# Kernel optimization log

Measured on AMD Instinct MI355X. Metric: run time of the kernel, lower is better.

Reference implementation:

```python
import jax, jax.numpy as jnp
import numpy as np

K = 9
HEADS = 4

def _inorm(x, axes):
    # torch InstanceNorm (affine=False, eps=1e-5, biased variance)
    m = x.mean(axes, keepdims=True)
    v = ((x - m) ** 2).mean(axes, keepdims=True)
    return (x - m) * jax.lax.rsqrt(v + 1e-5)

def _lrelu(x):
    return jax.nn.leaky_relu(x, 0.2)

def _knn_idx(coords, k):
    # coords: [B, 2, N] -> idx of k nearest (excluding self): [B, N, k]
    pts = jnp.swapaxes(coords, 1, 2)  # [B, N, 2]
    sq = (pts ** 2).sum(-1)
    dist = sq[:, :, None] + sq[:, None, :] - 2.0 * jnp.einsum('bnc,bmc->bnm', pts, pts)
    dist = jnp.maximum(dist, 1e-12)
    _, idx = jax.lax.top_k(-dist, k + 1)  # smallest distances, sorted
    return idx[:, :, 1:]

def _gather_nb(feats, idx):
    # feats: [B, C, N], idx: [B, N, k] -> [B, C, N, k]
    return jnp.take_along_axis(feats[:, :, None, :], idx[:, None, :, :], axis=3)

def _graph_feature(coords, feats, k):
    B, C, N = feats.shape
    idx = _knn_idx(coords, k)
    nb = _gather_nb(feats, idx)
    ctr = jnp.broadcast_to(feats[..., None], (B, C, N, k))
    return jnp.concatenate([ctr, nb - ctr], axis=1), idx  # [B, 2C, N, k]

def _annu(x, w1, b1, w2, b2):
    # conv (1,3) stride (1,3): non-overlapping windows 9 -> 3, then conv (1,3): 3 -> 1
    B, Ci, N, kk = x.shape
    x = x.reshape(B, Ci, N, kk // 3, 3)
    x = jnp.einsum('bcnwt,oct->bonw', x, w1) + b1[None, :, None, None]
    x = jax.nn.relu(_inorm(x, (2, 3)))
    x = jnp.einsum('bcnt,oct->bon', x, w2) + b2[None, :, None]
    return jax.nn.relu(_inorm(x[..., None], (2, 3)))  # [B, Co, N, 1]

def _cos(a, b):
    dot = (a * b).sum(1)
    return (dot / (jnp.sqrt((a ** 2).sum(1)) * jnp.sqrt((b ** 2).sum(1))))[:, None]

def _self_attn(coords, feats, p):
    B, C, N = feats.shape
    k = min(K, N - 1)
    x0 = feats[..., None]
    x1_old, idx1 = _graph_feature(coords, feats, k)
    x1 = _annu(x1_old, p['a1w1'], p['a1b1'], p['a1w2'], p['a1b2'])
    ctr = jnp.broadcast_to(coords[..., None], coords.shape + (k,))  # [B,2,N,k]
    nei1 = _gather_nb(coords, idx1)
    f_ang1 = _annu(_cos(ctr, nei1), p['gw1'], p['gb1'], p['gw2'], p['gb2'])
    x2_cat, idx2 = _graph_feature(coords, x1[..., 0], k)
    x2 = _annu(x2_cat, p['a2w1'], p['a2b1'], p['a2w2'], p['a2b2'])
    nei2 = _gather_nb(coords, idx2)
    f_ang2 = _annu(_cos(ctr, nei2), p['gw1'], p['gb1'], p['gw2'], p['gb2'])
    x3 = jnp.concatenate([x0, x1 + f_ang1, x2 + f_ang2], axis=1)
    x3 = _lrelu(_inorm(jnp.einsum('oc,bcnk->bonk', p['conv3_w'], x3), (2, 3))).reshape(B, -1, N)
    x1o = _lrelu(_inorm(jnp.einsum('oc,bcnk->bonk', p['conv1_w'], x1_old), (2, 3))).max(-1, keepdims=True)
    x2o_cat, _ = _graph_feature(coords, x1o[..., 0], k)
    x2o = _lrelu(_inorm(jnp.einsum('oc,bcnk->bonk', p['conv2_w'], x2o_cat), (2, 3))).max(-1, keepdims=True)
    x3o = jnp.concatenate([x0, x1o, x2o], axis=1)
    x3o = _lrelu(_inorm(jnp.einsum('oc,bcnk->bonk', p['conv3o_w'], x3o), (2, 3))).reshape(B, -1, N)
    return x3 + x3o

def _mha(q_in, k_in, v_in, p):
    B, D, N = q_in.shape
    dim = D // HEADS
    def proj(x, w, b):
        return (jnp.einsum('oc,bcn->bon', w, x) + b[None, :, None]).reshape(B, dim, HEADS, -1)
    q = proj(q_in, p['wq'], p['bq'])
    kk = proj(k_in, p['wk'], p['bk'])
    v = proj(v_in, p['wv'], p['bv'])
    scores = jnp.einsum('bdhn,bdhm->bhnm', q, kk) / jnp.sqrt(jnp.float32(dim))
    prob = jax.nn.softmax(scores, axis=-1)
    x = jnp.einsum('bhnm,bdhm->bdhn', prob, v).reshape(B, D, -1)
    return jnp.einsum('oc,bcn->bon', p['wm'], x) + p['bm'][None, :, None]

def _attn_prop(x, source, p):
    msg = _mha(x, source, source, p)
    h = jnp.concatenate([x, msg], axis=1)
    h = jnp.einsum('oc,bcn->bon', p['mw1'], h) + p['mb1'][None, :, None]
    h = jax.nn.relu(_inorm(h, (2,)))
    return jnp.einsum('oc,bcn->bon', p['mw2'], h) + p['mb2'][None, :, None]

def setup_inputs() -> dict:
    key = jax.random.key(0)
    ks = iter(jax.random.split(key, 40))
    def rn(shape, s=0.1):
        return jax.random.normal(next(ks), shape, jnp.float32) * s
    B, C, N = 2, 128, 2048
    return {
        'desc0': rn((B, C, N), 1.0), 'desc1': rn((B, C, N), 1.0),
        'coords0': rn((B, 2, N), 1.0), 'coords1': rn((B, 2, N), 1.0),
        'sa_conv1_w': rn((C, 2 * C)), 'sa_conv2_w': rn((2 * C, 2 * C)),
        'sa_conv3_w': rn((C, 3 * C)), 'sa_conv3o_w': rn((C, 4 * C)),
        'sa_a1w1': rn((C, 2 * C, 3)), 'sa_a1b1': rn((C,)), 'sa_a1w2': rn((C, C, 3)), 'sa_a1b2': rn((C,)),
        'sa_a2w1': rn((C, 2 * C, 3)), 'sa_a2b1': rn((C,)), 'sa_a2w2': rn((C, C, 3)), 'sa_a2b2': rn((C,)),
        'sa_gw1': rn((C, 1, 3)), 'sa_gb1': rn((C,)), 'sa_gw2': rn((C, C, 3)), 'sa_gb2': rn((C,)),
        'ca_wq': rn((C, C)), 'ca_bq': rn((C,)), 'ca_wk': rn((C, C)), 'ca_bk': rn((C,)),
        'ca_wv': rn((C, C)), 'ca_bv': rn((C,)), 'ca_wm': rn((C, C)), 'ca_bm': rn((C,)),
        'ca_mw1': rn((2 * C, 2 * C)), 'ca_mb1': rn((2 * C,)), 'ca_mw2': rn((C, 2 * C)), 'ca_mb2': rn((C,)),
    }

def reference(desc0, desc1, coords0, coords1, sa_conv1_w, sa_conv2_w, sa_conv3_w, sa_conv3o_w, sa_a1w1, sa_a1b1, sa_a1w2, sa_a1b2, sa_a2w1, sa_a2b1, sa_a2w2, sa_a2b2, sa_gw1, sa_gb1, sa_gw2, sa_gb2, ca_wq, ca_bq, ca_wk, ca_bk, ca_wv, ca_bv, ca_wm, ca_bm, ca_mw1, ca_mb1, ca_mw2, ca_mb2):
    sp = dict(conv1_w=sa_conv1_w, conv2_w=sa_conv2_w, conv3_w=sa_conv3_w, conv3o_w=sa_conv3o_w,
              a1w1=sa_a1w1, a1b1=sa_a1b1, a1w2=sa_a1w2, a1b2=sa_a1b2,
              a2w1=sa_a2w1, a2b1=sa_a2b1, a2w2=sa_a2w2, a2b2=sa_a2b2,
              gw1=sa_gw1, gb1=sa_gb1, gw2=sa_gw2, gb2=sa_gb2)
    cp = dict(wq=ca_wq, bq=ca_bq, wk=ca_wk, bk=ca_bk, wv=ca_wv, bv=ca_bv, wm=ca_wm, bm=ca_bm,
              mw1=ca_mw1, mb1=ca_mb1, mw2=ca_mw2, mb2=ca_mb2)
    # layer_names = ['self', 'cross']
    desc0 = _self_attn(coords0, desc0, sp)
    desc1 = _self_attn(coords1, desc1, sp)
    desc0 = desc0 + _attn_prop(desc0, desc1, cp)
    desc1 = desc1 + _attn_prop(desc1, desc0, cp)
    return (desc0, desc1)
```

## Files before the change

### kernel.cpp

```cpp
#include <hip/hip_runtime.h>
#include <cfloat>
#include <math.h>

#define NPTS 2048
#define R2   8192
#define SPLITK 8

typedef __attribute__((ext_vector_type(8))) short bfrag;
typedef __attribute__((ext_vector_type(4))) float f32x4;

__device__ inline ushort f2bf(float f) {
  unsigned u = __float_as_uint(f);
  return (ushort)((u + 0x7fffu + ((u >> 16) & 1u)) >> 16);
}

__global__ __launch_bounds__(256) void prologue(
    const float* __restrict__ conv1, const float* __restrict__ conv2,
    const float* __restrict__ a1w1, const float* __restrict__ a1w2,
    const float* __restrict__ a2w1, const float* __restrict__ a2w2,
    const float* __restrict__ gw2,
    const float* __restrict__ wk, const float* __restrict__ bk,
    const float* __restrict__ wv, const float* __restrict__ bv,
    float* __restrict__ dwA1, float* __restrict__ a1w2r,
    float* __restrict__ dwA2, float* __restrict__ a2w2r,
    float* __restrict__ gw2r, float* __restrict__ dwC1, float* __restrict__ dwC2,
    float* __restrict__ wkv, float* __restrict__ bkv,
    const float* __restrict__ in0, const float* __restrict__ in1, float* __restrict__ FT,
    const float* __restrict__ P0, const float* __restrict__ P1,
    int* __restrict__ idx, float* __restrict__ cosv)
{
  int bid = blockIdx.x, tid = threadIdx.x;
  if (bid < 256) {
    int i = bid * 256 + tid;
    if (i < 512*128) {
      int row = i >> 7, c = i & 127;
      float v1, v2;
      if (row < 128) {
        float s1 = 0.f, s2 = 0.f;
        for (int t = 0; t < 3; t++) {
          s1 += a1w1[(row*256 + c)*3 + t] - a1w1[(row*256 + 128 + c)*3 + t];
          s2 += a2w1[(row*256 + c)*3 + t] - a2w1[(row*256 + 128 + c)*3 + t];
        }
        v1 = s1; v2 = s2;
      } else {
        int t = (row - 128) >> 7, o = row & 127;
        v1 = a1w1[(o*256 + 128 + c)*3 + t];
        v2 = a2w1[(o*256 + 128 + c)*3 + t];
      }
      dwA1[i] = v1; dwA2[i] = v2;
      dwC2[i] = (row < 256) ? (conv2[row*256 + c] - conv2[row*256 + 128 + c])
                            : conv2[(row-256)*256 + 128 + c];
    }
    if (i < 128*384) {
      int o = i / 384, rem = i % 384, w = rem >> 7, c = rem & 127;
      a1w2r[i] = a1w2[(o*128 + c)*3 + w];
      a2w2r[i] = a2w2[(o*128 + c)*3 + w];
      gw2r[i]  = gw2[(o*128 + c)*3 + w];
    }
    if (i < 256*128) {
      int row = i >> 7, c = i & 127;
      dwC1[i] = (row < 128) ? (conv1[row*256 + c] - conv1[row*256 + 128 + c])
                            : conv1[(row-128)*256 + 128 + c];
      wkv[i] = (row < 128) ? wk[row*128 + c] : wv[(row-128)*128 + c];
    }
    if (i < 256) bkv[i] = (i < 128) ? bk[i] : bv[i - 128];
    return;
  }
  if (bid < 1280) {
    __shared__ float tile[32][33];
    int q = bid - 256;
    int zb = q >> 8, rem = q & 255, by = rem >> 6, bx = rem & 63;
    const float* src = (zb < 2) ? (in0 + (size_t)zb*128*2048) : (in1 + (size_t)(zb-2)*128*2048);
    float* dst = FT + (size_t)zb*2048*128;
    int i0 = by * 32, j0 = bx * 32;
    int tx = tid & 31, ty = tid >> 5;
    for (int s = 0; s < 32; s += 8)
      tile[ty + s][tx] = src[(size_t)(i0 + ty + s)*2048 + (j0 + tx)];
    __syncthreads();
    for (int s = 0; s < 32; s += 8)
      dst[(size_t)(j0 + ty + s)*128 + (i0 + tx)] = tile[tx][ty + s];
    return;
  }
  {
    __shared__ float px[NPTS], py[NPTS], sq[NPTS];
    int gw = (bid - 1280) * 4 + (tid >> 6);
    int b4 = gw >> 11, n = gw & 2047;
    int lane = tid & 63;
    const float* Pb = (b4 < 2) ? (P0 + (size_t)b4 * 2 * NPTS) : (P1 + (size_t)(b4 - 2) * 2 * NPTS);
    for (int i = tid; i < NPTS; i += 256) {
      float x = Pb[i], y = Pb[NPTS + i];
      px[i] = x; py[i] = y;
      sq[i] = __fadd_rn(__fmul_rn(x, x), __fmul_rn(y, y));
    }
    __syncthreads();
    float xn = px[n], yn = py[n], sqn = sq[n];
    float d32[32];
#pragma unroll
    for (int j = 0; j < 32; j++) {
      int m = lane + j*64;
      float dot  = __fadd_rn(__fmul_rn(xn, px[m]), __fmul_rn(yn, py[m]));
      float dist = __fsub_rn(__fadd_rn(sqn, sq[m]), __fmul_rn(2.0f, dot));
      d32[j] = fmaxf(dist, 1e-12f);
    }
    for (int r = 0; r < 10; r++) {
      float bv2 = d32[0]; int bj = 0;
#pragma unroll
      for (int j = 1; j < 32; j++) {
        bool lt = d32[j] < bv2;
        bv2 = lt ? d32[j] : bv2;
        bj = lt ? j : bj;
      }
      float wvv = bv2;
      int   wii = lane + bj*64;
      for (int off = 32; off >= 1; off >>= 1) {
        float od = __shfl_xor(wvv, off);
        int   oi = __shfl_xor(wii, off);
        if (od < wvv || (od == wvv && oi < wii)) { wvv = od; wii = oi; }
      }
      if (r > 0 && lane == 0) {
        size_t base = (size_t)gw*9 + (r - 1);
        idx[base] = wii;
        float dot = __fadd_rn(__fmul_rn(xn, px[wii]), __fmul_rn(yn, py[wii]));
        cosv[base] = __fdiv_rn(dot, __fmul_rn(__fsqrt_rn(sqn), __fsqrt_rn(sq[wii])));
      }
      if ((wii & 63) == lane) {
        int wj = wii >> 6;
#pragma unroll
        for (int j = 0; j < 32; j++) if (j == wj) d32[j] = FLT_MAX;
      }
    }
  }
}

__global__ void transpose_k(const float* __restrict__ in, float* __restrict__ out, int I, int J) {
  __shared__ float tile[32][33];
  int b = blockIdx.z;
  int i0 = blockIdx.y * 32, j0 = blockIdx.x * 32;
  int tx = threadIdx.x, ty = threadIdx.y;
  for (int s = 0; s < 32; s += 8)
    tile[ty + s][tx] = in[((size_t)b*I + (i0 + ty + s))*J + (j0 + tx)];
  __syncthreads();
  for (int s = 0; s < 32; s += 8)
    out[((size_t)b*J + (j0 + ty + s))*I + (i0 + tx)] = tile[tx][ty + s];
}

template<int BM>
__device__ __forceinline__ void gemm_body(
    const float* __restrict__ p0, int w0, const float* __restrict__ st0, int a0, int xm0,
    const float* __restrict__ p1, int w1, const float* __restrict__ st1, int a1, int xm1,
    const float* __restrict__ p2, int w2, const float* __restrict__ st2, int a2, int xm2,
    const float* __restrict__ addp, const float* __restrict__ addst,
    const float* __restrict__ W, const float* __restrict__ bias,
    const float* __restrict__ resid,
    float* __restrict__ Y, int Cin, int O, int pack, float* __restrict__ Y2,
    float* __restrict__ part,
    int r0, int c0, int pbx)
{
  __shared__ ushort Xs[BM][40];
  __shared__ ushort Ws[64][40];
  constexpr int RT = BM / 16;
  constexpr int XF = BM / 8;
  int tid = threadIdx.x;
  int wv = tid >> 6, l = tid & 63;
  int m16 = l & 15, kq = l >> 4;
  int sxr = tid & (BM - 1), sxc = (tid / BM) * XF;
  int swr = tid & 63, swc = (tid >> 6) * 8;
  f32x4 acc[RT];
#pragma unroll
  for (int t = 0; t < RT; t++) acc[t] = (f32x4){0.f, 0.f, 0.f, 0.f};
  for (int k0 = 0; k0 < Cin; k0 += 32) {
    {
      int r = r0 + sxr;
      int ac = k0 + sxc;
      const float* P; const float* st; int cc, lw, act, xm;
      if (ac < w0)            { P = p0; cc = ac;          lw = w0; st = st0; act = a0; xm = xm0; }
      else if (ac < w0 + w1)  { P = p1; cc = ac - w0;     lw = w1; st = st1; act = a1; xm = xm1; }
      else                    { P = p2; cc = ac - w0 - w1; lw = w2; st = st2; act = a2; xm = xm2; }
      float vv[XF];
#pragma unroll
      for (int q = 0; q < XF; q += 4)
        *(float4*)&vv[q] = *(const float4*)(P + (size_t)r*lw + cc + q);
      int b = r >> 11;
      if (st) {
#pragma unroll
        for (int j = 0; j < XF; j++) {
          int o = (cc + j) & (xm - 1);
          float m = st[(b*xm + o)*2], rs = st[(b*xm + o)*2 + 1];
          float v = (vv[j] - m) * rs;
          vv[j] = (act == 1) ? fmaxf(v, 0.f) : ((v >= 0.f) ? v : 0.2f*v);
        }
      }
      if (addp && ac >= 128) {
        int fc = (ac - 128) & 127;
        float av[XF];
#pragma unroll
        for (int q = 0; q < XF; q += 4)
          *(float4*)&av[q] = *(const float4*)(addp + (size_t)r*128 + fc + q);
        if (addst) {
#pragma unroll
          for (int j = 0; j < XF; j++) {
            int o = (fc + j) & 127;
            float m = addst[(b*128 + o)*2], rs = addst[(b*128 + o)*2 + 1];
            av[j] = fmaxf((av[j] - m) * rs, 0.f);
          }
        }
#pragma unroll
        for (int j = 0; j < XF; j++) vv[j] += av[j];
      }
      union { ushort u[XF]; ushort4 v4[XF/4]; } pk;
#pragma unroll
      for (int j = 0; j < XF; j++) pk.u[j] = f2bf(vv[j]);
#pragma unroll
      for (int q = 0; q < XF/4; q++) *(ushort4*)&Xs[sxr][sxc + q*4] = pk.v4[q];
    }
    {
      const float* s = W + (size_t)(c0 + swr)*Cin + k0 + swc;
      float4 v0 = *(const float4*)s, v1 = *(const float4*)(s + 4);
      union { ushort u[8]; ushort4 v4[2]; } pk;
      pk.u[0]=f2bf(v0.x); pk.u[1]=f2bf(v0.y); pk.u[2]=f2bf(v0.z); pk.u[3]=f2bf(v0.w);
      pk.u[4]=f2bf(v1.x); pk.u[5]=f2bf(v1.y); pk.u[6]=f2bf(v1.z); pk.u[7]=f2bf(v1.w);
      *(ushort4*)&Ws[swr][swc]     = pk.v4[0];
      *(ushort4*)&Ws[swr][swc + 4] = pk.v4[1];
    }
    __syncthreads();
    bfrag bf = *(const bfrag*)&Ws[wv*16 + m16][kq*8];
#pragma unroll
    for (int t = 0; t < RT; t++) {
      bfrag af = *(const bfrag*)&Xs[t*16 + m16][kq*8];
      acc[t] = __builtin_amdgcn_mfma_f32_16x16x32_bf16(af, bf, acc[t], 0, 0, 0);
    }
    __syncthreads();
  }
  int c = c0 + wv*16 + m16;
  float bi = bias ? bias[c] : 0.f;
  float ps = 0.f, ps2 = 0.f;
#pragma unroll
  for (int t = 0; t < RT; t++) {
#pragma unroll
    for (int i = 0; i < 4; i++) {
      int r = r0 + t*16 + kq*4 + i;
      float v = acc[t][i] + bi;
      if (resid) v += resid[(size_t)r*O + c];
      if (pack) {
        int cc2 = c & 127;
        int h = cc2 & 3, dd = cc2 >> 2, b = r >> 11, n = r & 2047;
        float* T = (pack == 1 || c < 128) ? Y : Y2;
        T[(((size_t)(b*4 + h))*NPTS + n)*32 + dd] = v;
      } else {
        Y[(size_t)r*O + c] = v;
      }
      ps += v; ps2 = fmaf(v, v, ps2);
    }
  }
  if (part) {
    ps  += __shfl_xor(ps, 16);  ps  += __shfl_xor(ps, 32);
    ps2 += __shfl_xor(ps2, 16); ps2 += __shfl_xor(ps2, 32);
    if (kq == 0) {
      part[((size_t)pbx*O + c)*2]     = ps;
      part[((size_t)pbx*O + c)*2 + 1] = ps2;
    }
  }
}

template<int BM>
__global__ __launch_bounds__(256) void gemm_m(
    const float* __restrict__ p0, int w0, const float* __restrict__ st0, int a0, int xm0,
    const float* __restrict__ p1, int w1, const float* __restrict__ st1, int a1, int xm1,
    const float* __restrict__ p2, int w2, const float* __restrict__ st2, int a2, int xm2,
    const float* __restrict__ addp, const float* __restrict__ addst,
    const float* __restrict__ W, const float* __restrict__ bias,
    const float* __restrict__ resid,
    float* __restrict__ Y, int Cin, int O, int pack, float* __restrict__ Y2,
    float* __restrict__ part)
{
  gemm_body<BM>(p0,w0,st0,a0,xm0, p1,w1,st1,a1,xm1, p2,w2,st2,a2,xm2,
                addp,addst, W,bias,resid, Y,Cin,O,pack,Y2,part,
                blockIdx.x*BM, blockIdx.y*64, blockIdx.x);
}

__global__ __launch_bounds__(256) void gemm_qkv(
    const float* __restrict__ Xbase,
    const float* __restrict__ wq, const float* __restrict__ bq, float* __restrict__ Qo,
    const float* __restrict__ wkv, const float* __restrict__ bkv, float* __restrict__ Ko,
    float* __restrict__ Vo)
{
  int bx = blockIdx.x, by = blockIdx.y;
  if (bx < 128) {
    if (by >= 2) return;
    gemm_body<32>(Xbase,128,nullptr,0,0, nullptr,0,nullptr,0,0, nullptr,0,nullptr,0,0,
                  nullptr,nullptr, wq, bq, nullptr, Qo, 128, 128, 1, nullptr, nullptr,
                  bx*32, by*64, 0);
  } else {
    gemm_body<32>(Xbase + (size_t)4096*128,128,nullptr,0,0, nullptr,0,nullptr,0,0, nullptr,0,nullptr,0,0,
                  nullptr,nullptr, wkv, bkv, nullptr, Ko, 128, 256, 2, Vo, nullptr,
                  (bx-128)*32, by*64, 0);
  }
}

__global__ __launch_bounds__(256) void combine_annu(const float* __restrict__ GA, const int* __restrict__ idx,
                                                    const float* __restrict__ b1, float* __restrict__ A,
                                                    double* __restrict__ part) {
  int t = threadIdx.x;
  int o = t & 127, sub = t >> 7;
  int r0 = blockIdx.x * 4;
  __shared__ int nbs[4][9];
  if (t < 36) nbs[t / 9][t % 9] = idx[(size_t)(r0 + t/9)*9 + (t % 9)];
  __syncthreads();
  float bo = b1[o];
  double s = 0.0, s2 = 0.0;
  for (int rr = sub; rr < 4; rr += 2) {
    int r = r0 + rr, rb = r & ~2047;
    float ctr = GA[(size_t)r*512 + o] + bo;
#pragma unroll
    for (int w = 0; w < 3; w++) {
      float acc = ctr;
#pragma unroll
      for (int t3 = 0; t3 < 3; t3++) {
        int m = nbs[rr][w*3 + t3];
        acc += GA[(size_t)(rb + m)*512 + 128 + t3*128 + o];
      }
      A[(size_t)r*384 + w*128 + o] = acc;
      s += (double)acc; s2 += (double)acc * (double)acc;
    }
  }
  __shared__ double ls[256], ls2[256];
  ls[t] = s; ls2[t] = s2;
  __syncthreads();
  if (sub == 0) {
    s += ls[128 + o]; s2 += ls2[128 + o];
    part[((size_t)blockIdx.x*128 + o)*2] = s;
    part[((size_t)blockIdx.x*128 + o)*2 + 1] = s2;
  }
}

__global__ __launch_bounds__(256) void stats_cos(const float* __restrict__ partf, float* __restrict__ stat,
                                                 const float* __restrict__ cosv, const float* __restrict__ gw1,
                                                 const float* __restrict__ gb1, float* __restrict__ ANG,
                                                 double* __restrict__ part2) {
  int bid = blockIdx.x, t = threadIdx.x;
  if (bid < 64) {
    int g = bid * 8 + (t >> 5);
    int lane = t & 31;
    if (g >= 512) return;
    int b = g >> 7, o = g & 127;
    double S = 0.0, S2 = 0.0;
    for (int u = lane; u < 64; u += 32) {
      size_t blk = (size_t)(b*64 + u);
      S  += (double)partf[(blk*128 + o)*2];
      S2 += (double)partf[(blk*128 + o)*2 + 1];
    }
    for (int off = 16; off >= 1; off >>= 1) {
      S  += __shfl_down(S, off, 32);
      S2 += __shfl_down(S2, off, 32);
    }
    if (lane == 0) {
      double mean = S / 2048;
      double var = S2 / 2048 - mean*mean;
      if (var < 0.0) var = 0.0;
      stat[g*2] = (float)mean;
      stat[g*2 + 1] = (float)(1.0 / sqrt(var + 1e-5));
    }
    return;
  }
  {
    int cbid = bid - 64;
    int o = t & 127, sub = t >> 7;
    int r0 = cbid * 16;
    float g0 = gw1[o*3], g1 = gw1[o*3+1], g2 = gw1[o*3+2], gb = gb1[o];
    __shared__ float cs[16][12];
    for (int i = t; i < 16*9; i += 256) cs[i / 9][i % 9] = cosv[(size_t)(r0 + i/9)*9 + (i % 9)];
    __syncthreads();
    double s = 0.0, s2 = 0.0;
    for (int rr = sub; rr < 16; rr += 2) {
      int r = r0 + rr;
#pragma unroll
      for (int w = 0; w < 3; w++) {
        float acc = gb;
        acc += cs[rr][w*3+0]*g0;
        acc += cs[rr][w*3+1]*g1;
        acc += cs[rr][w*3+2]*g2;
        ANG[(size_t)r*384 + w*128 + o] = acc;
        s += (double)acc; s2 += (double)acc * (double)acc;
      }
    }
    __shared__ double ls[256], ls2[256];
    ls[t] = s; ls2[t] = s2;
    __syncthreads();
    if (sub == 0) {
      s += ls[128 + o]; s2 += ls2[128 + o];
      part2[((size_t)cbid*128 + o)*2] = s;
      part2[((size_t)cbid*128 + o)*2 + 1] = s2;
    }
  }
}

__global__ __launch_bounds__(256) void gm_final(const double* __restrict__ part, float* __restrict__ stats,
                                                int Cc, int NB, int nblk, int count) {
  int g = blockIdx.x * 8 + (threadIdx.x >> 5);
  int lane = threadIdx.x & 31;
  if (g >= NB*Cc) return;
  int b = g / Cc, o = g % Cc;
  double S = 0.0, S2 = 0.0;
  for (int u = lane; u < nblk; u += 32) {
    size_t blk = (size_t)(b*nblk + u);
    S  += part[(blk*Cc + o)*2];
    S2 += part[(blk*Cc + o)*2 + 1];
  }
  for (int off = 16; off >= 1; off >>= 1) {
    S  += __shfl_down(S, off, 32);
    S2 += __shfl_down(S2, off, 32);
  }
  if (lane == 0) {
    double mean = S / count;
    double var = S2 / count - mean*mean;
    if (var < 0.0) var = 0.0;
    stats[g*2] = (float)mean;
    stats[g*2 + 1] = (float)(1.0 / sqrt(var + 1e-5));
  }
}

__global__ __launch_bounds__(256) void gm_final_f(const float* __restrict__ part, float* __restrict__ stats,
                                                  int Cc, int NB, int nblk, int count) {
  int g = blockIdx.x * 8 + (threadIdx.x >> 5);
  int lane = threadIdx.x & 31;
  if (g >= NB*Cc) return;
  int b = g / Cc, o = g % Cc;
  double S = 0.0, S2 = 0.0;
  for (int u = lane; u < nblk; u += 32) {
    size_t blk = (size_t)(b*nblk + u);
    S  += (double)part[(blk*Cc + o)*2];
    S2 += (double)part[(blk*Cc + o)*2 + 1];
  }
  for (int off = 16; off >= 1; off >>= 1) {
    S  += __shfl_down(S, off, 32);
    S2 += __shfl_down(S2, off, 32);
  }
  if (lane == 0) {
    double mean = S / count;
    double var = S2 / count - mean*mean;
    if (var < 0.0) var = 0.0;
    stats[g*2] = (float)mean;
    stats[g*2 + 1] = (float)(1.0 / sqrt(var + 1e-5));
  }
}

__global__ __launch_bounds__(256) void gather_max_partial(const float* __restrict__ G, const int* __restrict__ idx,
                                                          float* __restrict__ maxbuf, double* __restrict__ part,
                                                          int Cc) {
  int t = threadIdx.x;
  int o = t % Cc, sub = t / Cc, nsub = 256 / Cc;
  int r0 = blockIdx.x * 4;
  __shared__ int nbs[4][9];
  if (t < 36) nbs[t / 9][t % 9] = idx[(size_t)(r0 + t/9)*9 + (t % 9)];
  __syncthreads();
  double s = 0.0, s2 = 0.0;
  for (int rr = sub; rr < 4; rr += nsub) {
    int r = r0 + rr, rb = r & ~2047;
    float g = G[(size_t)r*2*Cc + o];
    float mx = -3.4e38f;
#pragma unroll
    for (int k = 0; k < 9; k++) {
      int m = nbs[rr][k];
      float v = g + G[(size_t)(rb + m)*2*Cc + Cc + o];
      mx = fmaxf(mx, v); s += (double)v; s2 += (double)v*(double)v;
    }
    maxbuf[(size_t)r*Cc + o] = mx;
  }
  if (nsub == 2) {
    __shared__ double ls[256], ls2[256];
    ls[t] = s; ls2[t] = s2;
    __syncthreads();
    if (sub == 0) { s += ls[Cc + o]; s2 += ls2[Cc + o]; }
  }
  if (sub == 0) {
    part[((size_t)blockIdx.x*Cc + o)*2] = s;
    part[((size_t)blockIdx.x*Cc + o)*2 + 1] = s2;
  }
}

__global__ void norm_add2(const float* __restrict__ src, float* __restrict__ dst,
                          const float* __restrict__ stats,
                          const float* __restrict__ addend, const float* __restrict__ astats,
                          int total) {
  int i = blockIdx.x * 256 + threadIdx.x;
  if (i >= total) return;
  int o = i & 127;
  int b = i >> 18;
  float m = stats[(b*128 + o)*2], rs = stats[(b*128 + o)*2 + 1];
  float v = (src[i] - m) * rs;
  v = (v >= 0.f) ? v : 0.2f*v;
  float ma = astats[(b*128 + o)*2], rsa = astats[(b*128 + o)*2 + 1];
  float a = (addend[i] - ma) * rsa;
  a = (a >= 0.f) ? a : 0.2f*a;
  dst[i] = v + a;
}

__global__ __launch_bounds__(256) void attn_part(const float* __restrict__ Qp, const float* __restrict__ Kp,
                                                 const float* __restrict__ Vp,
                                                 float* __restrict__ OP, float* __restrict__ ML) {
  __shared__ ushort Ks[64][40];
  __shared__ ushort Vt[32][72];
  __shared__ ushort Pb[64][72];
  int tid = threadIdx.x;
  int wv = tid >> 6, l = tid & 63;
  int d = l & 15, g = l >> 4;
  int kp = blockIdx.y, bh = blockIdx.z;
  int q0 = blockIdx.x * 64;
  const float* Qh = Qp + (size_t)bh * NPTS * 32;
  const float* Kh = Kp + (size_t)bh * NPTS * 32;
  const float* Vh = Vp + (size_t)bh * NPTS * 32;
  {
    int r = tid >> 2, c8 = (tid & 3) * 8;
    const float* q = Qh + (size_t)(q0 + r)*32 + c8;
    float4 v0 = *(const float4*)q, v1 = *(const float4*)(q + 4);
    union { ushort u[8]; ushort4 v4[2]; } pk;
    pk.u[0]=f2bf(v0.x); pk.u[1]=f2bf(v0.y); pk.u[2]=f2bf(v0.z); pk.u[3]=f2bf(v0.w);
    pk.u[4]=f2bf(v1.x); pk.u[5]=f2bf(v1.y); pk.u[6]=f2bf(v1.z); pk.u[7]=f2bf(v1.w);
    *(ushort4*)&Pb[r][c8]     = pk.v4[0];
    *(ushort4*)&Pb[r][c8 + 4] = pk.v4[1];
  }
  __syncthreads();
  bfrag qf = *(const bfrag*)&Pb[wv*16 + d][g*8];
  f32x4 Oc[2];
  Oc[0] = (f32x4){0.f,0.f,0.f,0.f}; Oc[1] = (f32x4){0.f,0.f,0.f,0.f};
  float m_[4] = {-FLT_MAX, -FLT_MAX, -FLT_MAX, -FLT_MAX};
  float l_[4] = {0.f, 0.f, 0.f, 0.f};
  const float sc = 0.17677669529663687f;
  int ks0 = kp * (NPTS / SPLITK);
  for (int k0 = ks0; k0 < ks0 + NPTS/SPLITK; k0 += 64) {
    __syncthreads();
    {
      int r = tid >> 2, c8 = (tid & 3) * 8;
      const float* kr = Kh + (size_t)(k0 + r)*32 + c8;
      float4 a0 = *(const float4*)kr, a1 = *(const float4*)(kr + 4);
      union { ushort u[8]; ushort4 v4[2]; } pk;
      pk.u[0]=f2bf(a0.x); pk.u[1]=f2bf(a0.y); pk.u[2]=f2bf(a0.z); pk.u[3]=f2bf(a0.w);
      pk.u[4]=f2bf(a1.x); pk.u[5]=f2bf(a1.y); pk.u[6]=f2bf(a1.z); pk.u[7]=f2bf(a1.w);
      *(ushort4*)&Ks[r][c8]     = pk.v4[0];
      *(ushort4*)&Ks[r][c8 + 4] = pk.v4[1];
      int vr = tid & 63, vd = (tid >> 6) * 8;
      const float* vp = Vh + (size_t)(k0 + vr)*32 + vd;
      float4 b0 = *(const float4*)vp, b1 = *(const float4*)(vp + 4);
      Vt[vd+0][vr] = f2bf(b0.x); Vt[vd+1][vr] = f2bf(b0.y);
      Vt[vd+2][vr] = f2bf(b0.z); Vt[vd+3][vr] = f2bf(b0.w);
      Vt[vd+4][vr] = f2bf(b1.x); Vt[vd+5][vr] = f2bf(b1.y);
      Vt[vd+6][vr] = f2bf(b1.z); Vt[vd+7][vr] = f2bf(b1.w);
    }
    __syncthreads();
    f32x4 S[4];
#pragma unroll
    for (int c = 0; c < 4; c++) {
      S[c] = (f32x4){0.f,0.f,0.f,0.f};
      bfrag kf = *(const bfrag*)&Ks[c*16 + d][g*8];
      S[c] = __builtin_amdgcn_mfma_f32_16x16x32_bf16(qf, kf, S[c], 0, 0, 0);
    }
    float cf[4];
#pragma unroll
    for (int i = 0; i < 4; i++) {
      float tm = fmaxf(fmaxf(S[0][i], S[1][i]), fmaxf(S[2][i], S[3][i])) * sc;
      for (int off = 1; off < 16; off <<= 1) tm = fmaxf(tm, __shfl_xor(tm, off));
      float mn = fmaxf(m_[i], tm);
      cf[i] = __expf(m_[i] - mn);
      m_[i] = mn;
    }
    float rs[4] = {0.f, 0.f, 0.f, 0.f};
    ushort pu[4][4];
#pragma unroll
    for (int c = 0; c < 4; c++)
#pragma unroll
      for (int i = 0; i < 4; i++) {
        float p = __expf(fmaf(S[c][i], sc, -m_[i]));
        rs[i] += p;
        pu[c][i] = f2bf(p);
      }
#pragma unroll
    for (int i = 0; i < 4; i++) {
      float r2 = rs[i];
      for (int off = 1; off < 16; off <<= 1) r2 += __shfl_xor(r2, off);
      l_[i] = l_[i]*cf[i] + r2;
      Oc[0][i] *= cf[i]; Oc[1][i] *= cf[i];
    }
#pragma unroll
    for (int c = 0; c < 4; c++)
#pragma unroll
      for (int i = 0; i < 4; i++)
        Pb[wv*16 + g*4 + i][c*16 + d] = pu[c][i];
#pragma unroll
    for (int s5 = 0; s5 < 2; s5++) {
      bfrag pf = *(const bfrag*)&Pb[wv*16 + d][g*8 + 32*s5];
#pragma unroll
      for (int td = 0; td < 2; td++) {
        union { ushort4 v4[2]; bfrag f; } vu;
        vu.v4[0] = *(const ushort4*)&Vt[td*16 + d][g*8 + 32*s5];
        vu.v4[1] = *(const ushort4*)&Vt[td*16 + d][g*8 + 32*s5 + 4];
        Oc[td] = __builtin_amdgcn_mfma_f32_16x16x32_bf16(pf, vu.f, Oc[td], 0, 0, 0);
      }
    }
  }
  size_t pb = (size_t)(kp*8 + bh) * NPTS;
#pragma unroll
  for (int i = 0; i < 4; i++) {
    int n = q0 + wv*16 + g*4 + i;
    OP[(pb + n)*32 + d]      = Oc[0][i];
    OP[(pb + n)*32 + 16 + d] = Oc[1][i];
    if (d == 0) { ML[(pb + n)*2] = m_[i]; ML[(pb + n)*2 + 1] = l_[i]; }
  }
}

__global__ void attn_merge(const float* __restrict__ OP, const float* __restrict__ ML,
                           float* __restrict__ out) {
  int i = blockIdx.x * 256 + threadIdx.x;
  if (i >= 8*2048*16) return;
  int dp = (i & 15) * 2;
  int n  = (i >> 4) & 2047;
  int bh = i >> 15;
  float mv[SPLITK], lv[SPLITK];
  float mm = -FLT_MAX;
#pragma unroll
  for (int p = 0; p < SPLITK; p++) {
    size_t pp = ((size_t)(p*8 + bh) * NPTS + n);
    mv[p] = ML[pp*2]; lv[p] = ML[pp*2 + 1];
    mm = fmaxf(mm, mv[p]);
  }
  float L = 0.f, ox = 0.f, oy = 0.f;
#pragma unroll
  for (int p = 0; p < SPLITK; p++) {
    size_t pp = ((size_t)(p*8 + bh) * NPTS + n);
    float w = __expf(mv[p] - mm);
    L += w * lv[p];
    float2 o = *(const float2*)&OP[pp*32 + dp];
    ox += w * o.x; oy += w * o.y;
  }
  float inv = 1.f / L;
  int b = bh >> 2, h = bh & 3;
  out[((size_t)(b*NPTS + n))*128 + (dp+0)*4 + h] = ox * inv;
  out[((size_t)(b*NPTS + n))*128 + (dp+1)*4 + h] = oy * inv;
}

extern "C" void kernel_launch(void* const* d_in, const int* in_sizes, int n_in,
                              void* d_out, int out_size, void* d_ws, size_t ws_size,
                              hipStream_t stream) {
  (void)in_sizes; (void)n_in; (void)out_size; (void)ws_size;
  const float* desc0  = (const float*)d_in[0];
  const float* desc1  = (const float*)d_in[1];
  const float* coords0= (const float*)d_in[2];
  const float* coords1= (const float*)d_in[3];
  const float* conv1w = (const float*)d_in[4];
  const float* conv2w = (const float*)d_in[5];
  const float* conv3w = (const float*)d_in[6];
  const float* conv3ow= (const float*)d_in[7];
  const float* a1w1 = (const float*)d_in[8];
  const float* a1b1 = (const float*)d_in[9];
  const float* a1w2 = (const float*)d_in[10];
  const float* a1b2 = (const float*)d_in[11];
  const float* a2w1 = (const float*)d_in[12];
  const float* a2b1 = (const float*)d_in[13];
  const float* a2w2 = (const float*)d_in[14];
  const float* a2b2 = (const float*)d_in[15];
  const float* gw1  = (const float*)d_in[16];
  const float* gb1  = (const float*)d_in[17];
  const float* gw2  = (const float*)d_in[18];
  const float* gb2  = (const float*)d_in[19];
  const float* wq = (const float*)d_in[20]; const float* bq = (const float*)d_in[21];
  const float* wk = (const float*)d_in[22]; const float* bk = (const float*)d_in[23];
  const float* wv = (const float*)d_in[24]; const float* bv = (const float*)d_in[25];
  const float* wm = (const float*)d_in[26]; const float* bm = (const float*)d_in[27];
  const float* mw1 = (const float*)d_in[28]; const float* mb1 = (const float*)d_in[29];
  const float* mw2 = (const float*)d_in[30]; const float* mb2 = (const float*)d_in[31];

  float* ws = (float*)d_ws;
  size_t off = 0;
  auto alloc = [&](size_t nel) { size_t r = off; off += (nel + 63) & ~(size_t)63; return r; };
  float* DW_A1 = ws + alloc(512*128);
  float* W_A1R = ws + alloc(128*384);
  float* DW_A2 = ws + alloc(512*128);
  float* W_A2R = ws + alloc(128*384);
  float* W_G2R = ws + alloc(128*384);
  float* DW_C1 = ws + alloc(256*128);
  float* DW_C2 = ws + alloc(512*128);
  float* W_KV  = ws + alloc(256*128);
  float* B_KV  = ws + alloc(256);
  float* SA   = ws + alloc((size_t)R2*128);
  float* XF0  = ws + alloc((size_t)4096*128);
  float* XF1  = ws + alloc((size_t)4096*128);
  int*   IDX  = (int*)(ws + alloc((size_t)R2*9));
  float* COSV = ws + alloc((size_t)R2*9);
  float* FT   = ws + alloc((size_t)R2*128);
  float* BIG  = ws + alloc((size_t)R2*512);
  float* ABUF = ws + alloc((size_t)R2*384);
  float* X1B  = ws + alloc((size_t)R2*128);
  float* FANG = ws + alloc((size_t)R2*128);
  float* X2B  = ws + alloc((size_t)R2*128);
  float* X3A  = ws + alloc((size_t)R2*128);
  float* X1O  = ws + alloc((size_t)R2*128);
  float* AB2  = ws + alloc((size_t)R2*256);
  float* X3O  = ws + alloc((size_t)R2*128);
  double* PART = (double*)(ws + alloc((size_t)2048*256*2*2));
  float*  PARTF = (float*)PART;
  double* PART2 = PART + (size_t)512*1024;
  float* STATS = ws + alloc(8*2048);
  float* MLB  = ws + alloc((size_t)SPLITK*8*NPTS*2);
  float* ST_T   = STATS;
  float* ST_X1B = STATS + 2048;
  float* ST_FANG= STATS + 4096;
  float* ST_X2B = STATS + 6144;
  float* ST_X3A = STATS + 8192;
  float* ST_X1O = STATS + 10240;
  float* ST_AB  = STATS + 12288;
  float* ST_X3O = STATS + 14336;
  float* OP  = BIG;

  auto g64 = [&](const float* p0,int w0,const float* st0,int a0,int x0,
                 const float* p1,int w1,const float* st1,int a1,int x1,
                 const float* p2,int w2,const float* st2,int a2,int x2,
                 const float* addp,const float* addst,
                 const float* W,const float* bias,const float* resid,
                 float* Y,int R,int Cin,int O,int pack,float* Y2,float* part) {
    gemm_m<64><<<dim3(R/64, O/64), 256, 0, stream>>>(p0,w0,st0,a0,x0, p1,w1,st1,a1,x1,
        p2,w2,st2,a2,x2, addp,addst, W,bias,resid, Y,Cin,O,pack,Y2,part);
  };
  auto g32 = [&](const float* p0,int w0,const float* st0,int a0,int x0,
                 const float* p1,int w1,const float* st1,int a1,int x1,
                 const float* p2,int w2,const float* st2,int a2,int x2,
                 const float* addp,const float* addst,
                 const float* W,const float* bias,const float* resid,
                 float* Y,int R,int Cin,int O,int pack,float* Y2,float* part) {
    gemm_m<32><<<dim3(R/32, O/64), 256, 0, stream>>>(p0,w0,st0,a0,x0, p1,w1,st1,a1,x1,
        p2,w2,st2,a2,x2, addp,addst, W,bias,resid, Y,Cin,O,pack,Y2,part);
  };
  auto statsF = [&](float* stat, int O, int NB, int nblk, int count) {
    gm_final_f<<<(NB*O + 7)/8, 256, 0, stream>>>(PARTF, stat, O, NB, nblk, count);
  };
  auto statsD = [&](float* stat, int O, int NB, int nblk, int count) {
    gm_final<<<(NB*O + 7)/8, 256, 0, stream>>>(PART, stat, O, NB, nblk, count);
  };
  auto gathermax = [&](const float* G, float* mx, int Cc, float* stat) {
    gather_max_partial<<<R2/4, 256, 0, stream>>>(G, IDX, mx, PART, Cc);
    statsD(stat, Cc, 4, 512, 2048*9);
  };

  prologue<<<3328, 256, 0, stream>>>(conv1w, conv2w, a1w1, a1w2, a2w1, a2w2, gw2,
                                     wk, bk, wv, bv,
                                     DW_A1, W_A1R, DW_A2, W_A2R, W_G2R, DW_C1, DW_C2,
                                     W_KV, B_KV,
                                     desc0, desc1, FT,
                                     coords0, coords1, IDX, COSV);

  g64(FT,128,nullptr,0,0, nullptr,0,nullptr,0,0, nullptr,0,nullptr,0,0, nullptr,nullptr,
      DW_A1, nullptr, nullptr, BIG, R2, 128, 512, 0, nullptr, nullptr);
  combine_annu<<<R2/4, 256, 0, stream>>>(BIG, IDX, a1b1, ABUF, PART);
  statsD(ST_T, 128, 4, 512, 2048*3);
  g32(ABUF,384,ST_T,1,128, nullptr,0,nullptr,0,0, nullptr,0,nullptr,0,0, nullptr,nullptr,
      W_A1R, a1b2, nullptr, X1B, R2, 384, 128, 0, nullptr, PARTF);
  stats_cos<<<64 + R2/16, 256, 0, stream>>>(PARTF, ST_X1B, COSV, gw1, gb1, ABUF, PART2);
  gm_final<<<(4*128 + 7)/8, 256, 0, stream>>>(PART2, ST_T, 128, 4, 128, 2048*3);
  g32(ABUF,384,ST_T,1,128, nullptr,0,nullptr,0,0, nullptr,0,nullptr,0,0, nullptr,nullptr,
      W_G2R, gb2, nullptr, FANG, R2, 384, 128, 0, nullptr, PARTF);
  statsF(ST_FANG, 128, 4, 64, 2048);
  g64(X1B,128,ST_X1B,1,128, nullptr,0,nullptr,0,0, nullptr,0,nullptr,0,0, nullptr,nullptr,
      DW_A2, nullptr, nullptr, BIG, R2, 128, 512, 0, nullptr, nullptr);
  combine_annu<<<R2/4, 256, 0, stream>>>(BIG, IDX, a2b1, ABUF, PART);
  statsD(ST_T, 128, 4, 512, 2048*3);
  g32(ABUF,384,ST_T,1,128, nullptr,0,nullptr,0,0, nullptr,0,nullptr,0,0, nullptr,nullptr,
      W_A2R, a2b2, nullptr, X2B, R2, 384, 128, 0, nullptr, PARTF);
  statsF(ST_X2B, 128, 4, 64, 2048);
  g32(FT,128,nullptr,0,0, X1B,128,ST_X1B,1,128, X2B,128,ST_X2B,1,128, FANG,ST_FANG,
      conv3w, nullptr, nullptr, X3A, R2, 384, 128, 0, nullptr, PARTF);
  statsF(ST_X3A, 128, 4, 64, 2048);
  g64(FT,128,nullptr,0,0, nullptr,0,nullptr,0,0, nullptr,0,nullptr,0,0, nullptr,nullptr,
      DW_C1, nullptr, nullptr, BIG, R2, 128, 256, 0, nullptr, nullptr);
  gathermax(BIG, X1O, 128, ST_X1O);
  g64(X1O,128,ST_X1O,2,128, nullptr,0,nullptr,0,0, nullptr,0,nullptr,0,0, nullptr,nullptr,
      DW_C2, nullptr, nullptr, BIG, R2, 128, 512, 0, nullptr, nullptr);
  gathermax(BIG, AB2, 256, ST_AB);
  g32(FT,128,nullptr,0,0, X1O,128,ST_X1O,2,128, AB2,256,ST_AB,2,256, nullptr,nullptr,
      conv3ow, nullptr, nullptr, X3O, R2, 512, 128, 0, nullptr, PARTF);
  statsF(ST_X3O, 128, 4, 64, 2048);
  norm_add2<<<(R2*128 + 255)/256, 256, 0, stream>>>(X3O, SA, ST_X3O, X3A, ST_X3A, R2*128);

  float* SA1 = SA + (size_t)4096*128;
  auto prop = [&](const float* xbase, float* dst) {
    const float* xin = xbase;
    gemm_qkv<<<dim3(256, 4), 256, 0, stream>>>(xbase, wq, bq, X1B, W_KV, B_KV, X2B, X3A);
    attn_part<<<dim3(2048/64, SPLITK, 8), 256, 0, stream>>>(X1B, X2B, X3A, OP, MLB);
    attn_merge<<<(8*2048*16 + 255)/256, 256, 0, stream>>>(OP, MLB, FANG);
    g32(FANG,128,nullptr,0,0, nullptr,0,nullptr,0,0, nullptr,0,nullptr,0,0, nullptr,nullptr,
        wm, bm, nullptr, X1O, 4096, 128, 128, 0, nullptr, nullptr);
    g32(xin,128,nullptr,0,0, X1O,128,nullptr,0,0, nullptr,0,nullptr,0,0, nullptr,nullptr,
        mw1, mb1, nullptr, ABUF, 4096, 256, 256, 0, nullptr, PARTF);
    statsF(ST_T, 256, 2, 64, 2048);
    g32(ABUF,256,ST_T,1,256, nullptr,0,nullptr,0,0, nullptr,0,nullptr,0,0, nullptr,nullptr,
        mw2, mb2, xin, dst, 4096, 256, 128, 0, nullptr, nullptr);
  };

  prop(SA, XF0);
  prop(SA1, XF1);

  transpose_k<<<dim3(128/32, 2048/32, 2), dim3(32, 8), 0, stream>>>(XF0, (float*)d_out, 2048, 128);
  transpose_k<<<dim3(128/32, 2048/32, 2), dim3(32, 8), 0, stream>>>(XF1, (float*)d_out + (size_t)4096*128, 2048, 128);
}
```

Baseline: 468.0 us.

## Fuse norm-stat finalization into GEMM epilogue and streamline kNN argmin

Each GEMM that produces per-block partial sums now finalizes the instance-norm mean and rstd itself. It does this with a last-block-done atomic counter, which removes the separate gm_final_f and stats launches. The kNN selection keeps each lane's running minimum and rescans its 32 registers only in the lane that owned the extracted winner, instead of every lane rescanning every round. The two output transposes merge into one launch, and stats_cos is reduced to a cos_conv kernel followed by the generic stats reduction. In exchange, the stats reduction runs on a single trailing block with serial per-thread loops, and the code adds counter memsets and threadfence overhead.

```diff
diff --git a/kernel.cpp b/kernel.cpp
--- a/kernel.cpp
+++ b/kernel.cpp
@@ -102,14 +102,14 @@
       float dist = __fsub_rn(__fadd_rn(sqn, sq[m]), __fmul_rn(2.0f, dot));
       d32[j] = fmaxf(dist, 1e-12f);
     }
+    float bv2 = d32[0]; int bj = 0;
+#pragma unroll
+    for (int j = 1; j < 32; j++) {
+      bool lt = d32[j] < bv2;
+      bv2 = lt ? d32[j] : bv2;
+      bj = lt ? j : bj;
+    }
     for (int r = 0; r < 10; r++) {
-      float bv2 = d32[0]; int bj = 0;
-#pragma unroll
-      for (int j = 1; j < 32; j++) {
-        bool lt = d32[j] < bv2;
-        bv2 = lt ? d32[j] : bv2;
-        bj = lt ? j : bj;
-      }
       float wvv = bv2;
       int   wii = lane + bj*64;
       for (int off = 32; off >= 1; off >>= 1) {
@@ -127,6 +127,13 @@
         int wj = wii >> 6;
 #pragma unroll
         for (int j = 0; j < 32; j++) if (j == wj) d32[j] = FLT_MAX;
+        bv2 = d32[0]; bj = 0;
+#pragma unroll
+        for (int j = 1; j < 32; j++) {
+          bool lt = d32[j] < bv2;
+          bv2 = lt ? d32[j] : bv2;
+          bj = lt ? j : bj;
+        }
       }
     }
   }
@@ -154,7 +161,8 @@
     const float* __restrict__ resid,
     float* __restrict__ Y, int Cin, int O, int pack, float* __restrict__ Y2,
     float* __restrict__ part,
-    int r0, int c0, int pbx)
+    int r0, int c0, int pbx,
+    float* __restrict__ statout, int NB, int* __restrict__ ctr)
 {
   __shared__ ushort Xs[BM][40];
   __shared__ ushort Ws[64][40];
@@ -259,6 +267,30 @@
       part[((size_t)pbx*O + c)*2]     = ps;
       part[((size_t)pbx*O + c)*2 + 1] = ps2;
     }
+    if (statout) {
+      __threadfence();
+      __syncthreads();
+      __shared__ int lastBlk;
+      if (tid == 0) lastBlk = (atomicAdd(ctr, 1) == (int)(gridDim.x*gridDim.y) - 1) ? 1 : 0;
+      __syncthreads();
+      if (!lastBlk) return;
+      __threadfence();
+      int nblk = (int)gridDim.x / NB;
+      for (int p = tid; p < NB*O; p += 256) {
+        int b = p / O, o = p % O;
+        double S = 0.0, S2 = 0.0;
+        for (int u = 0; u < nblk; u++) {
+          size_t base = (((size_t)(b*nblk + u))*O + o)*2;
+          S  += (double)part[base];
+          S2 += (double)part[base + 1];
+        }
+        double mean = S / 2048;
+        double var = S2 / 2048 - mean*mean;
+        if (var < 0.0) var = 0.0;
+        statout[p*2] = (float)mean;
+        statout[p*2 + 1] = (float)(1.0 / sqrt(var + 1e-5));
+      }
+    }
   }
 }
 
@@ -271,11 +303,11 @@
     const float* __restrict__ W, const float* __restrict__ bias,
     const float* __restrict__ resid,
     float* __restrict__ Y, int Cin, int O, int pack, float* __restrict__ Y2,
-    float* __restrict__ part)
+    float* __restrict__ part, float* __restrict__ statout, int NB, int* __restrict__ ctr)
 {
   gemm_body<BM>(p0,w0,st0,a0,xm0, p1,w1,st1,a1,xm1, p2,w2,st2,a2,xm2,
                 addp,addst, W,bias,resid, Y,Cin,O,pack,Y2,part,
-                blockIdx.x*BM, blockIdx.y*64, blockIdx.x);
+                blockIdx.x*BM, blockIdx.y*64, blockIdx.x, statout, NB, ctr);
 }
 
 __global__ __launch_bounds__(256) void gemm_qkv(
@@ -289,11 +321,11 @@
     if (by >= 2) return;
     gemm_body<32>(Xbase,128,nullptr,0,0, nullptr,0,nullptr,0,0, nullptr,0,nullptr,0,0,
                   nullptr,nullptr, wq, bq, nullptr, Qo, 128, 128, 1, nullptr, nullptr,
-                  bx*32, by*64, 0);
+                  bx*32, by*64, 0, nullptr, 0, nullptr);
   } else {
     gemm_body<32>(Xbase + (size_t)4096*128,128,nullptr,0,0, nullptr,0,nullptr,0,0, nullptr,0,nullptr,0,0,
                   nullptr,nullptr, wkv, bkv, nullptr, Ko, 128, 256, 2, Vo, nullptr,
-                  (bx-128)*32, by*64, 0);
+                  (bx-128)*32, by*64, 0, nullptr, 0, nullptr);
   }
 }
 
@@ -333,64 +365,36 @@
   }
 }
 
-__global__ __launch_bounds__(256) void stats_cos(const float* __restrict__ partf, float* __restrict__ stat,
-                                                 const float* __restrict__ cosv, const float* __restrict__ gw1,
-                                                 const float* __restrict__ gb1, float* __restrict__ ANG,
-                                                 double* __restrict__ part2) {
-  int bid = blockIdx.x, t = threadIdx.x;
-  if (bid < 64) {
-    int g = bid * 8 + (t >> 5);
-    int lane = t & 31;
-    if (g >= 512) return;
-    int b = g >> 7, o = g & 127;
-    double S = 0.0, S2 = 0.0;
-    for (int u = lane; u < 64; u += 32) {
-      size_t blk = (size_t)(b*64 + u);
-      S  += (double)partf[(blk*128 + o)*2];
-      S2 += (double)partf[(blk*128 + o)*2 + 1];
-    }
-    for (int off = 16; off >= 1; off >>= 1) {
-      S  += __shfl_down(S, off, 32);
-      S2 += __shfl_down(S2, off, 32);
-    }
-    if (lane == 0) {
-      double mean = S / 2048;
-      double var = S2 / 2048 - mean*mean;
-      if (var < 0.0) var = 0.0;
-      stat[g*2] = (float)mean;
-      stat[g*2 + 1] = (float)(1.0 / sqrt(var + 1e-5));
-    }
-    return;
-  }
-  {
-    int cbid = bid - 64;
-    int o = t & 127, sub = t >> 7;
-    int r0 = cbid * 16;
-    float g0 = gw1[o*3], g1 = gw1[o*3+1], g2 = gw1[o*3+2], gb = gb1[o];
-    __shared__ float cs[16][12];
-    for (int i = t; i < 16*9; i += 256) cs[i / 9][i % 9] = cosv[(size_t)(r0 + i/9)*9 + (i % 9)];
-    __syncthreads();
-    double s = 0.0, s2 = 0.0;
-    for (int rr = sub; rr < 16; rr += 2) {
-      int r = r0 + rr;
-#pragma unroll
-      for (int w = 0; w < 3; w++) {
-        float acc = gb;
-        acc += cs[rr][w*3+0]*g0;
-        acc += cs[rr][w*3+1]*g1;
-        acc += cs[rr][w*3+2]*g2;
-        ANG[(size_t)r*384 + w*128 + o] = acc;
-        s += (double)acc; s2 += (double)acc * (double)acc;
-      }
-    }
-    __shared__ double ls[256], ls2[256];
-    ls[t] = s; ls2[t] = s2;
-    __syncthreads();
-    if (sub == 0) {
-      s += ls[128 + o]; s2 += ls2[128 + o];
-      part2[((size_t)cbid*128 + o)*2] = s;
-      part2[((size_t)cbid*128 + o)*2 + 1] = s2;
-    }
+__global__ __launch_bounds__(256) void cos_conv(const float* __restrict__ cosv, const float* __restrict__ gw1,
+                                                const float* __restrict__ gb1, float* __restrict__ ANG,
+                                                double* __restrict__ part) {
+  int t = threadIdx.x;
+  int o = t & 127, sub = t >> 7;
+  int r0 = blockIdx.x * 16;
+  float g0 = gw1[o*3], g1 = gw1[o*3+1], g2 = gw1[o*3+2], gb = gb1[o];
+  __shared__ float cs[16][12];
+  for (int i = t; i < 16*9; i += 256) cs[i / 9][i % 9] = cosv[(size_t)(r0 + i/9)*9 + (i % 9)];
+  __syncthreads();
+  double s = 0.0, s2 = 0.0;
+  for (int rr = sub; rr < 16; rr += 2) {
+    int r = r0 + rr;
+#pragma unroll
+    for (int w = 0; w < 3; w++) {
+      float acc = gb;
+      acc += cs[rr][w*3+0]*g0;
+      acc += cs[rr][w*3+1]*g1;
+      acc += cs[rr][w*3+2]*g2;
+      ANG[(size_t)r*384 + w*128 + o] = acc;
+      s += (double)acc; s2 += (double)acc * (double)acc;
+    }
+  }
+  __shared__ double ls[256], ls2[256];
+  ls[t] = s; ls2[t] = s2;
+  __syncthreads();
+  if (sub == 0) {
+    s += ls[128 + o]; s2 += ls2[128 + o];
+    part[((size_t)blockIdx.x*128 + o)*2] = s;
+    part[((size_t)blockIdx.x*128 + o)*2 + 1] = s2;
   }
 }
 
@@ -405,31 +409,6 @@
     size_t blk = (size_t)(b*nblk + u);
     S  += part[(blk*Cc + o)*2];
     S2 += part[(blk*Cc + o)*2 + 1];
-  }
-  for (int off = 16; off >= 1; off >>= 1) {
-    S  += __shfl_down(S, off, 32);
-    S2 += __shfl_down(S2, off, 32);
-  }
-  if (lane == 0) {
-    double mean = S / count;
-    double var = S2 / count - mean*mean;
-    if (var < 0.0) var = 0.0;
-    stats[g*2] = (float)mean;
-    stats[g*2 + 1] = (float)(1.0 / sqrt(var + 1e-5));
-  }
-}
-
-__global__ __launch_bounds__(256) void gm_final_f(const float* __restrict__ part, float* __restrict__ stats,
-                                                  int Cc, int NB, int nblk, int count) {
-  int g = blockIdx.x * 8 + (threadIdx.x >> 5);
-  int lane = threadIdx.x & 31;
-  if (g >= NB*Cc) return;
-  int b = g / Cc, o = g % Cc;
-  double S = 0.0, S2 = 0.0;
-  for (int u = lane; u < nblk; u += 32) {
-    size_t blk = (size_t)(b*nblk + u);
-    S  += (double)part[(blk*Cc + o)*2];
-    S2 += (double)part[(blk*Cc + o)*2 + 1];
   }
   for (int off = 16; off >= 1; off >>= 1) {
     S  += __shfl_down(S, off, 32);
@@ -697,9 +676,9 @@
   float* X3O  = ws + alloc((size_t)R2*128);
   double* PART = (double*)(ws + alloc((size_t)2048*256*2*2));
   float*  PARTF = (float*)PART;
-  double* PART2 = PART + (size_t)512*1024;
   float* STATS = ws + alloc(8*2048);
   float* MLB  = ws + alloc((size_t)SPLITK*8*NPTS*2);
+  int*   CTR  = (int*)(ws + alloc(64));
   float* ST_T   = STATS;
   float* ST_X1B = STATS + 2048;
   float* ST_FANG= STATS + 4096;
@@ -710,26 +689,28 @@
   float* ST_X3O = STATS + 14336;
   float* OP  = BIG;
 
+  hipMemsetAsync(CTR, 0, 64*sizeof(int), stream);
+  int ctr_id = 0;
+
   auto g64 = [&](const float* p0,int w0,const float* st0,int a0,int x0,
                  const float* p1,int w1,const float* st1,int a1,int x1,
                  const float* p2,int w2,const float* st2,int a2,int x2,
                  const float* addp,const float* addst,
                  const float* W,const float* bias,const float* resid,
-                 float* Y,int R,int Cin,int O,int pack,float* Y2,float* part) {
+                 float* Y,int R,int Cin,int O,int pack,float* Y2,float* part,float* statout) {
     gemm_m<64><<<dim3(R/64, O/64), 256, 0, stream>>>(p0,w0,st0,a0,x0, p1,w1,st1,a1,x1,
-        p2,w2,st2,a2,x2, addp,addst, W,bias,resid, Y,Cin,O,pack,Y2,part);
+        p2,w2,st2,a2,x2, addp,addst, W,bias,resid, Y,Cin,O,pack,Y2,part,
+        statout, R/2048, statout ? (CTR + ctr_id++) : nullptr);
   };
   auto g32 = [&](const float* p0,int w0,const float* st0,int a0,int x0,
                  const float* p1,int w1,const float* st1,int a1,int x1,
                  const float* p2,int w2,const float* st2,int a2,int x2,
                  const float* addp,const float* addst,
                  const float* W,const float* bias,const float* resid,
-                 float* Y,int R,int Cin,int O,int pack,float* Y2,float* part) {
+                 float* Y,int R,int Cin,int O,int pack,float* Y2,float* part,float* statout) {
     gemm_m<32><<<dim3(R/32, O/64), 256, 0, stream>>>(p0,w0,st0,a0,x0, p1,w1,st1,a1,x1,
-        p2,w2,st2,a2,x2, addp,addst, W,bias,resid, Y,Cin,O,pack,Y2,part);
-  };
-  auto statsF = [&](float* stat, int O, int NB, int nblk, int count) {
-    gm_final_f<<<(NB*O + 7)/8, 256, 0, stream>>>(PARTF, stat, O, NB, nblk, count);
+        p2,w2,st2,a2,x2, addp,addst, W,bias,resid, Y,Cin,O,pack,Y2,part,
+        statout, R/2048, statout ? (CTR + ctr_id++) : nullptr);
   };
   auto statsD = [&](float* stat, int O, int NB, int nblk, int count) {
     gm_final<<<(NB*O + 7)/8, 256, 0, stream>>>(PART, stat, O, NB, nblk, count);
@@ -747,35 +728,31 @@
                                      coords0, coords1, IDX, COSV);
 
   g64(FT,128,nullptr,0,0, nullptr,0,nullptr,0,0, nullptr,0,nullptr,0,0, nullptr,nullptr,
-      DW_A1, nullptr, nullptr, BIG, R2, 128, 512, 0, nullptr, nullptr);
+      DW_A1, nullptr, nullptr, BIG, R2, 128, 512, 0, nullptr, nullptr, nullptr);
   combine_annu<<<R2/4, 256, 0, stream>>>(BIG, IDX, a1b1, ABUF, PART);
   statsD(ST_T, 128, 4, 512, 2048*3);
   g32(ABUF,384,ST_T,1,128, nullptr,0,nullptr,0,0, nullptr,0,nullptr,0,0, nullptr,nullptr,
-      W_A1R, a1b2, nullptr, X1B, R2, 384, 128, 0, nullptr, PARTF);
-  stats_cos<<<64 + R2/16, 256, 0, stream>>>(PARTF, ST_X1B, COSV, gw1, gb1, ABUF, PART2);
-  gm_final<<<(4*128 + 7)/8, 256, 0, stream>>>(PART2, ST_T, 128, 4, 128, 2048*3);
+      W_A1R, a1b2, nullptr, X1B, R2, 384, 128, 0, nullptr, PARTF, ST_X1B);
+  cos_conv<<<R2/16, 256, 0, stream>>>(COSV, gw1, gb1, ABUF, PART);
+  statsD(ST_T, 128, 4, 128, 2048*3);
   g32(ABUF,384,ST_T,1,128, nullptr,0,nullptr,0,0, nullptr,0,nullptr,0,0, nullptr,nullptr,
-      W_G2R, gb2, nullptr, FANG, R2, 384, 128, 0, nullptr, PARTF);
-  statsF(ST_FANG, 128, 4, 64, 2048);
+      W_G2R, gb2, nullptr, FANG, R2, 384, 128, 0, nullptr, PARTF, ST_FANG);
   g64(X1B,128,ST_X1B,1,128, nullptr,0,nullptr,0,0, nullptr,0,nullptr,0,0, nullptr,nullptr,
-      DW_A2, nullptr, nullptr, BIG, R2, 128, 512, 0, nullptr, nullptr);
+      DW_A2, nullptr, nullptr, BIG, R2, 128, 512, 0, nullptr, nullptr, nullptr);
   combine_annu<<<R2/4, 256, 0, stream>>>(BIG, IDX, a2b1, ABUF, PART);
   statsD(ST_T, 128, 4, 512, 2048*3);
   g32(ABUF,384,ST_T,1,128, nullptr,0,nullptr,0,0, nullptr,0,nullptr,0,0, nullptr,nullptr,
-      W_A2R, a2b2, nullptr, X2B, R2, 384, 128, 0, nullptr, PARTF);
-  statsF(ST_X2B, 128, 4, 64, 2048);
+      W_A2R, a2b2, nullptr, X2B, R2, 384, 128, 0, nullptr, PARTF, ST_X2B);
   g32(FT,128,nullptr,0,0, X1B,128,ST_X1B,1,128, X2B,128,ST_X2B,1,128, FANG,ST_FANG,
-      conv3w, nullptr, nullptr, X3A, R2, 384, 128, 0, nullptr, PARTF);
-  statsF(ST_X3A, 128, 4, 64, 2048);
+      conv3w, nullptr, nullptr, X3A, R2, 384, 128, 0, nullptr, PARTF, ST_X3A);
   g64(FT,128,nullptr,0,0, nullptr,0,nullptr,0,0, nullptr,0,nullptr,0,0, nullptr,nullptr,
-      DW_C1, nullptr, nullptr, BIG, R2, 128, 256, 0, nullptr, nullptr);
+      DW_C1, nullptr, nullptr, BIG, R2, 128, 256, 0, nullptr, nullptr, nullptr);
   gathermax(BIG, X1O, 128, ST_X1O);
   g64(X1O,128,ST_X1O,2,128, nullptr,0,nullptr,0,0, nullptr,0,nullptr,0,0, nullptr,nullptr,
-      DW_C2, nullptr, nullptr, BIG, R2, 128, 512, 0, nullptr, nullptr);
+      DW_C2, nullptr, nullptr, BIG, R2, 128, 512, 0, nullptr, nullptr, nullptr);
   gathermax(BIG, AB2, 256, ST_AB);
   g32(FT,128,nullptr,0,0, X1O,128,ST_X1O,2,128, AB2,256,ST_AB,2,256, nullptr,nullptr,
-      conv3ow, nullptr, nullptr, X3O, R2, 512, 128, 0, nullptr, PARTF);
-  statsF(ST_X3O, 128, 4, 64, 2048);
+      conv3ow, nullptr, nullptr, X3O, R2, 512, 128, 0, nullptr, PARTF, ST_X3O);
   norm_add2<<<(R2*128 + 255)/256, 256, 0, stream>>>(X3O, SA, ST_X3O, X3A, ST_X3A, R2*128);
 
   float* SA1 = SA + (size_t)4096*128;
@@ -785,17 +762,15 @@
     attn_part<<<dim3(2048/64, SPLITK, 8), 256, 0, stream>>>(X1B, X2B, X3A, OP, MLB);
     attn_merge<<<(8*2048*16 + 255)/256, 256, 0, stream>>>(OP, MLB, FANG);
     g32(FANG,128,nullptr,0,0, nullptr,0,nullptr,0,0, nullptr,0,nullptr,0,0, nullptr,nullptr,
-        wm, bm, nullptr, X1O, 4096, 128, 128, 0, nullptr, nullptr);
+        wm, bm, nullptr, X1O, 4096, 128, 128, 0, nullptr, nullptr, nullptr);
     g32(xin,128,nullptr,0,0, X1O,128,nullptr,0,0, nullptr,0,nullptr,0,0, nullptr,nullptr,
-        mw1, mb1, nullptr, ABUF, 4096, 256, 256, 0, nullptr, PARTF);
-    statsF(ST_T, 256, 2, 64, 2048);
+        mw1, mb1, nullptr, ABUF, 4096, 256, 256, 0, nullptr, PARTF, ST_T);
     g32(ABUF,256,ST_T,1,256, nullptr,0,nullptr,0,0, nullptr,0,nullptr,0,0, nullptr,nullptr,
-        mw2, mb2, xin, dst, 4096, 256, 128, 0, nullptr, nullptr);
+        mw2, mb2, xin, dst, 4096, 256, 128, 0, nullptr, nullptr, nullptr);
   };
 
   prop(SA, XF0);
   prop(SA1, XF1);
 
-  transpose_k<<<dim3(128/32, 2048/32, 2), dim3(32, 8), 0, stream>>>(XF0, (float*)d_out, 2048, 128);
-  transpose_k<<<dim3(128/32, 2048/32, 2), dim3(32, 8), 0, stream>>>(XF1, (float*)d_out + (size_t)4096*128, 2048, 128);
-}
+  transpose_k<<<dim3(128/32, 2048/32, 4), dim3(32, 8), 0, stream>>>(XF0, (float*)d_out, 2048, 128);
+}
```

Measured after the change: 974.1 us. 2.08x slower.
